# Optimization experiments

Measured on AMD Instinct MI355X. Metric: run time of the kernel, lower is better.

Reference implementation:

```python
import jax, jax.numpy as jnp
import numpy as np

OBS = 256      # observation_space_size == state_vector_len
SV = 2047      # STATE_VECTORS = WMG_MAX_OBS
D = 256        # tfm_vec_size = 8 heads * 32 head_size
H = 8
HD = 32
L = 2          # TFM_NUM_LAYERS
FF = 1024      # TFM_HIDDEN_SIZE
ACH = 512      # AC_HIDDEN_LAYER_SIZE
A = 16         # action_space_size


def setup_inputs() -> dict:
    key = jax.random.key(0)
    ks = jax.random.split(key, 24)
    r = lambda k, s: (jax.random.normal(k, s, jnp.float32) * 0.02)
    inp = {
        "observation": jax.random.normal(ks[0], (OBS,), jnp.float32),
        "old_vectors": jax.random.normal(ks[1], (SV, OBS), jnp.float32),
        "W_core": r(ks[2], (OBS, D)), "b_core": jnp.zeros((D,), jnp.float32),
        # memo embedding takes cat(state_vec, age_onehot) of size OBS+SV
        "W_memo": r(ks[3], (OBS + SV, D)), "b_memo": jnp.zeros((D,), jnp.float32),
        "Wq": r(ks[4], (L, D, D)), "bq": jnp.zeros((L, D), jnp.float32),
        "Wk": r(ks[5], (L, D, D)), "bk": jnp.zeros((L, D), jnp.float32),
        "Wv": r(ks[6], (L, D, D)), "bv": jnp.zeros((L, D), jnp.float32),
        "Wo": r(ks[7], (L, D, D)), "bo": jnp.zeros((L, D), jnp.float32),
        "ln1_g": jnp.ones((L, D), jnp.float32), "ln1_b": jnp.zeros((L, D), jnp.float32),
        "ln2_g": jnp.ones((L, D), jnp.float32), "ln2_b": jnp.zeros((L, D), jnp.float32),
        "W_ff1": r(ks[8], (L, D, FF)), "b_ff1": jnp.zeros((L, FF), jnp.float32),
        "W_ff2": r(ks[9], (L, FF, D)), "b_ff2": jnp.zeros((L, D), jnp.float32),
        "aW1": r(ks[10], (D, ACH)), "ab1": jnp.zeros((ACH,), jnp.float32),
        "aW2": r(ks[11], (ACH, ACH)), "ab2": jnp.zeros((ACH,), jnp.float32),
        "aWo": r(ks[12], (ACH, A)), "abo": jnp.zeros((A,), jnp.float32),
        "cW1": r(ks[13], (D, ACH)), "cb1": jnp.zeros((ACH,), jnp.float32),
        "cW2": r(ks[14], (ACH, ACH)), "cb2": jnp.zeros((ACH,), jnp.float32),
        "cWo": r(ks[15], (ACH, 1)), "cbo": jnp.zeros((1,), jnp.float32),
    }
    return inp


def _ln(x, g, b, eps=1e-5):
    m = jnp.mean(x, axis=-1, keepdims=True)
    v = jnp.mean(jnp.square(x - m), axis=-1, keepdims=True)
    return (x - m) * jax.lax.rsqrt(v + eps) * g + b


def reference(observation, old_vectors, W_core, b_core, W_memo, b_memo,
              Wq, bq, Wk, bk, Wv, bv, Wo, bo,
              ln1_g, ln1_b, ln2_g, ln2_b, W_ff1, b_ff1, W_ff2, b_ff2,
              aW1, ab1, aW2, ab2, aWo, abo, cW1, cb1, cW2, cb2, cWo, cbo):
    # core embedding [D]
    emb0 = observation @ W_core + b_core
    # fused memo + age-onehot embedding: cat(vec_i, e_i) @ W_memo == vec_i @ W_memo[:OBS] + W_memo[OBS+i]
    memo_emb = old_vectors @ W_memo[:OBS] + W_memo[OBS:] + b_memo  # [SV, D]
    x = jnp.concatenate([emb0[None, :], memo_emb], axis=0)[None]   # [1, 1+SV, D]
    S = 1 + SV
    scale = 1.0 / np.sqrt(HD).astype(np.float32)
    for l in range(L):
        q = (x @ Wq[l] + bq[l]).reshape(1, S, H, HD)
        k = (x @ Wk[l] + bk[l]).reshape(1, S, H, HD)
        v = (x @ Wv[l] + bv[l]).reshape(1, S, H, HD)
        scores = jnp.einsum('bqhd,bkhd->bhqk', q, k) * scale       # [1,H,S,S]
        probs = jax.nn.softmax(scores, axis=-1)
        ctx = jnp.einsum('bhqk,bkhd->bqhd', probs, v).reshape(1, S, D)
        x = _ln(x + ctx @ Wo[l] + bo[l], ln1_g[l], ln1_b[l])
        h = jax.nn.gelu(x @ W_ff1[l] + b_ff1[l])
        x = _ln(x + h @ W_ff2[l] + b_ff2[l], ln2_g[l], ln2_b[l])
    t = x[:, 0, :]                                                 # [1, D]
    ha = jnp.tanh(jnp.tanh(t @ aW1 + ab1) @ aW2 + ab2)
    policy = ha @ aWo + abo                                        # [1, A] logits
    hc = jnp.tanh(jnp.tanh(t @ cW1 + cb1) @ cW2 + cb2)
    value_est = hc @ cWo + cbo                                     # [1, 1]
    # WMG_MAX_MEMOS == 0 path: new state vector is tanh(observation)
    new_vector = jnp.tanh(observation)                             # [OBS]
    return value_est, policy, new_vector
```

## Files before the change

kernel.cpp:

```cpp
#include <hip/hip_runtime.h>
#include <stdint.h>

typedef __attribute__((ext_vector_type(8))) short bf16x8;
typedef __attribute__((ext_vector_type(4))) float f32x4;

constexpr int kSEQ = 2048;
constexpr int kD   = 256;
constexpr int kHD  = 32;
constexpr int kFF  = 1024;
constexpr int kA   = 16;

__device__ __forceinline__ unsigned short f2b(float f) {
  union { float f; unsigned int u; } v; v.f = f;
  unsigned int r = v.u + 0x7FFFu + ((v.u >> 16) & 1u);
  return (unsigned short)(r >> 16);
}

struct ConvTable {
  const float* src[13];
  int K[13];
  int N[13];
  int dst[13];
  int tstart[14];
};

union SharedU {
  struct { unsigned short lt[64][72]; } cv;
  struct { unsigned short Al[64][40]; unsigned short Bl[32][40]; } g64;
  struct { unsigned short Kl[64][40]; unsigned short Vt[32][72];
           unsigned short Pl[4][16][72]; } at;
};

struct MegaParams {
  ConvTable tab;
  const float *obs, *oldv, *Wcore, *bcore, *Wmemo0, *bmemo, *Wmemo2;
  const float *bq, *bk, *bv, *bo, *ln1g, *ln1b, *ln2g, *ln2b, *bff1, *bff2;
  const float *aW1, *ab1, *aW2, *ab2, *aWo, *abo;
  const float *cW1, *cb1, *cW2, *cb2, *cWo, *cbo;
  float* xf; unsigned short* xb;
  unsigned short *qb, *kb, *vb, *wT;
  float *pacc, *pml, *h1, *h2, *out;
  int oQKV[2], oWoT[2], oFF1[2], oFF2[2];
  int convJobs, nsplit, tpb;
};

__device__ void conv_job(const MegaParams& p, SharedU& sh, int job) {
  const int tid = threadIdx.x;
  if (job == p.convJobs) {
    float a = p.bcore[tid];
    #pragma unroll 8
    for (int k = 0; k < 256; k++) a += p.obs[k] * p.Wcore[k * kD + tid];
    p.xf[tid] = a;
    p.xb[tid] = f2b(a);
    return;
  }
  int m = 0;
  while (job >= p.tab.tstart[m + 1]) m++;
  const int tloc = job - p.tab.tstart[m];
  const int N = p.tab.N[m], K = p.tab.K[m];
  const int ntile = N >> 6;
  const int k0 = (tloc / ntile) * 64, n0 = (tloc % ntile) * 64;
  const float* src = p.tab.src[m];
  {
    const int r = tid >> 2, c16 = (tid & 3) * 16;
    const float* sp = src + (size_t)(k0 + r) * N + n0 + c16;
    #pragma unroll
    for (int j = 0; j < 16; j++) sh.cv.lt[r][c16 + j] = f2b(sp[j]);
  }
  __syncthreads();
  {
    const int n = tid >> 2, kc = (tid & 3) * 16;
    unsigned short* dp = p.wT + p.tab.dst[m] + (size_t)(n0 + n) * K + k0 + kc;
    unsigned short g[16];
    #pragma unroll
    for (int j = 0; j < 16; j++) g[j] = sh.cv.lt[kc + j][n];
    *(bf16x8*)dp = *(bf16x8*)&g[0];
    *(bf16x8*)(dp + 8) = *(bf16x8*)&g[8];
  }
}

__device__ void memo_job(const MegaParams& p, SharedU& sh, int job) {
  const int tid = threadIdx.x;
  const int w = tid >> 6, l = tid & 63, lg = l >> 4, lr = l & 15;
  const int sr = tid >> 2, sk = (tid & 3) * 8;
  const int kr = tid >> 3, nc = (tid & 7) * 4;
  const int m0 = (job & 31) * 64, n0 = (job >> 5) * 32;
  f32x4 acc[2];
  #pragma unroll
  for (int c = 0; c < 2; c++)
    #pragma unroll
    for (int i = 0; i < 4; i++) acc[c][i] = 0.f;

  auto loadA = [&](int k0) -> bf16x8 {
    bf16x8 av;
    if (m0 + sr < 2047) {
      const float* ap = p.oldv + (size_t)(m0 + sr) * 256 + k0 + sk;
      #pragma unroll
      for (int j = 0; j < 8; j++) av[j] = (short)f2b(ap[j]);
    } else {
      #pragma unroll
      for (int j = 0; j < 8; j++) av[j] = 0;
    }
    return av;
  };
  auto loadB = [&](int k0, float* b4) {
    const float* bp = p.Wmemo0 + (size_t)(k0 + kr) * kD + n0 + nc;
    #pragma unroll
    for (int j = 0; j < 4; j++) b4[j] = bp[j];
  };

  bf16x8 av = loadA(0);
  float b4[4];
  loadB(0, b4);

  for (int k0 = 0; k0 < 256; k0 += 32) {
    __syncthreads();
    *(bf16x8*)&sh.g64.Al[sr][sk] = av;
    #pragma unroll
    for (int j = 0; j < 4; j++) sh.g64.Bl[nc + j][kr] = f2b(b4[j]);
    __syncthreads();
    if (k0 + 32 < 256) {
      av = loadA(k0 + 32);
      loadB(k0 + 32, b4);
    }
    bf16x8 af = *(bf16x8*)&sh.g64.Al[w * 16 + lr][8 * lg];
    #pragma unroll
    for (int c = 0; c < 2; c++) {
      bf16x8 bf = *(bf16x8*)&sh.g64.Bl[c * 16 + lr][8 * lg];
      acc[c] = __builtin_amdgcn_mfma_f32_16x16x32_bf16(af, bf, acc[c], 0, 0, 0);
    }
  }

  #pragma unroll
  for (int c = 0; c < 2; c++)
    #pragma unroll
    for (int i = 0; i < 4; i++) {
      const int gr = m0 + w * 16 + 4 * lg + i;
      const int gc = n0 + c * 16 + lr;
      if (gr >= 2047) continue;
      const float v = acc[c][i] + p.bmemo[gc] + p.Wmemo2[(size_t)gr * kD + gc];
      p.xf[(size_t)(gr + 1) * kD + gc] = v;
      p.xb[(size_t)(gr + 1) * kD + gc] = f2b(v);
    }
}

__global__ __launch_bounds__(256) void k_cvm(MegaParams p) {
  __shared__ SharedU sh;
  if (blockIdx.x < 256) memo_job(p, sh, blockIdx.x);
  else conv_job(p, sh, blockIdx.x - 256);
}

__global__ __launch_bounds__(256) void k_qkv(MegaParams p, int lyr) {
  __shared__ SharedU sh;
  const int tid = threadIdx.x;
  const int w = tid >> 6, l = tid & 63, lg = l >> 4, lr = l & 15;
  const int sr = tid >> 2, sk = (tid & 3) * 8;
  const int job = blockIdx.x;
  const int m0 = (job & 31) * 64, n0 = (job >> 5) * 32;
  const unsigned short* BT = p.wT + p.oQKV[lyr];
  f32x4 acc[2];
  #pragma unroll
  for (int c = 0; c < 2; c++)
    #pragma unroll
    for (int i = 0; i < 4; i++) acc[c][i] = 0.f;

  bf16x8 av = *(const bf16x8*)(p.xb + (size_t)(m0 + sr) * 256 + sk);
  bf16x8 bv;
  if (tid < 128) bv = *(const bf16x8*)(BT + (size_t)(n0 + sr) * 256 + sk);

  for (int k0 = 0; k0 < 256; k0 += 32) {
    __syncthreads();
    *(bf16x8*)&sh.g64.Al[sr][sk] = av;
    if (tid < 128) *(bf16x8*)&sh.g64.Bl[sr][sk] = bv;
    __syncthreads();
    if (k0 + 32 < 256) {
      av = *(const bf16x8*)(p.xb + (size_t)(m0 + sr) * 256 + k0 + 32 + sk);
      if (tid < 128)
        bv = *(const bf16x8*)(BT + (size_t)(n0 + sr) * 256 + k0 + 32 + sk);
    }
    bf16x8 af = *(bf16x8*)&sh.g64.Al[w * 16 + lr][8 * lg];
    #pragma unroll
    for (int c = 0; c < 2; c++) {
      bf16x8 bf = *(bf16x8*)&sh.g64.Bl[c * 16 + lr][8 * lg];
      acc[c] = __builtin_amdgcn_mfma_f32_16x16x32_bf16(af, bf, acc[c], 0, 0, 0);
    }
  }

  #pragma unroll
  for (int c = 0; c < 2; c++)
    #pragma unroll
    for (int i = 0; i < 4; i++) {
      const int gr = m0 + w * 16 + 4 * lg + i;
      const int gc = n0 + c * 16 + lr;
      const int t = gc >> 8, cc = gc & 255;
      const float* bp = (t == 0) ? (p.bq + lyr * 256)
                        : (t == 1 ? (p.bk + lyr * 256) : (p.bv + lyr * 256));
      unsigned short* op = (t == 0) ? p.qb : (t == 1 ? p.kb : p.vb);
      float v = acc[c][i] + bp[cc];
      if (t == 0) v *= 0.17677669529663687f;
      op[(size_t)gr * kD + cc] = f2b(v);
    }
}

__device__ void attn_job(SharedU& sh, int qb_, int h, int s, int tpb,
                         const unsigned short* q, const unsigned short* k,
                         const unsigned short* v, float* pacc, float* pml) {
  const int tid = threadIdx.x;
  const int w = tid >> 6, l = tid & 63, lg = l >> 4, lr = l & 15;
  const int q0 = qb_ * 64;
  const int hoff = h * kHD;
  const int sr = tid >> 2, sk = (tid & 3) * 8;
  const int t0 = s * tpb;

  const bf16x8 qf =
      *(const bf16x8*)(q + (size_t)(q0 + w * 16 + lr) * kD + hoff + 8 * lg);

  float m_[4], l_[4];
  f32x4 acc[2];
  #pragma unroll
  for (int i = 0; i < 4; i++) { m_[i] = -1e30f; l_[i] = 0.f; }
  #pragma unroll
  for (int dt = 0; dt < 2; dt++)
    #pragma unroll
    for (int i = 0; i < 4; i++) acc[dt][i] = 0.f;

  bf16x8 kreg = *(const bf16x8*)(k + (size_t)(t0 * 64 + sr) * kD + hoff + sk);
  bf16x8 vreg = *(const bf16x8*)(v + (size_t)(t0 * 64 + sr) * kD + hoff + sk);

  for (int t = 0; t < tpb; t++) {
    __syncthreads();
    *(bf16x8*)&sh.at.Kl[sr][sk] = kreg;
    #pragma unroll
    for (int j = 0; j < 8; j++) sh.at.Vt[sk + j][sr] = (unsigned short)vreg[j];
    __syncthreads();
    if (t + 1 < tpb) {
      const size_t nx = (size_t)((t0 + t + 1) * 64 + sr) * kD + hoff + sk;
      kreg = *(const bf16x8*)(k + nx);
      vreg = *(const bf16x8*)(v + nx);
    }
    f32x4 sc[4];
    #pragma unroll
    for (int c = 0; c < 4; c++) {
      f32x4 z;
      #pragma unroll
      for (int i = 0; i < 4; i++) z[i] = 0.f;
      bf16x8 kf = *(bf16x8*)&sh.at.Kl[c * 16 + lr][8 * lg];
      sc[c] = __builtin_amdgcn_mfma_f32_16x16x32_bf16(qf, kf, z, 0, 0, 0);
    }
    float tm[4];
    #pragma unroll
    for (int i = 0; i < 4; i++)
      tm[i] = fmaxf(fmaxf(sc[0][i], sc[1][i]), fmaxf(sc[2][i], sc[3][i]));
    #pragma unroll
    for (int mm = 1; mm <= 8; mm <<= 1)
      #pragma unroll
      for (int i = 0; i < 4; i++) tm[i] = fmaxf(tm[i], __shfl_xor(tm[i], mm));
    float pv[4][4], rs[4], corr[4];
    #pragma unroll
    for (int i = 0; i < 4; i++) {
      const float nm = fmaxf(m_[i], tm[i]);
      corr[i] = __expf(m_[i] - nm);
      m_[i] = nm;
      rs[i] = 0.f;
    }
    #pragma unroll
    for (int c = 0; c < 4; c++)
      #pragma unroll
      for (int i = 0; i < 4; i++) {
        pv[c][i] = __expf(sc[c][i] - m_[i]);
        rs[i] += pv[c][i];
      }
    #pragma unroll
    for (int mm = 1; mm <= 8; mm <<= 1)
      #pragma unroll
      for (int i = 0; i < 4; i++) rs[i] += __shfl_xor(rs[i], mm);
    #pragma unroll
    for (int i = 0; i < 4; i++) {
      l_[i] = l_[i] * corr[i] + rs[i];
      acc[0][i] *= corr[i];
      acc[1][i] *= corr[i];
    }
    #pragma unroll
    for (int c = 0; c < 4; c++)
      #pragma unroll
      for (int i = 0; i < 4; i++)
        sh.at.Pl[w][4 * lg + i][c * 16 + lr] = f2b(pv[c][i]);
    __syncthreads();
    #pragma unroll
    for (int k2 = 0; k2 < 2; k2++) {
      bf16x8 pf_ = *(bf16x8*)&sh.at.Pl[w][lr][k2 * 32 + 8 * lg];
      #pragma unroll
      for (int dt = 0; dt < 2; dt++) {
        bf16x8 vf = *(bf16x8*)&sh.at.Vt[dt * 16 + lr][k2 * 32 + 8 * lg];
        acc[dt] = __builtin_amdgcn_mfma_f32_16x16x32_bf16(pf_, vf, acc[dt], 0, 0, 0);
      }
    }
  }

  const int pb = s * 8 + h;
  float* pa = pacc + (size_t)pb * kSEQ * kHD;
  float* pm = pml + (size_t)pb * kSEQ * 2;
  #pragma unroll
  for (int dt = 0; dt < 2; dt++)
    #pragma unroll
    for (int i = 0; i < 4; i++) {
      const int gr = q0 + w * 16 + 4 * lg + i;
      pa[(size_t)gr * kHD + dt * 16 + lr] = acc[dt][i];
    }
  if (lr == 0) {
    #pragma unroll
    for (int i = 0; i < 4; i++) {
      const int gr = q0 + w * 16 + 4 * lg + i;
      float2 ml; ml.x = m_[i]; ml.y = l_[i];
      *(float2*)&pm[(size_t)gr * 2] = ml;
    }
  }
}

__global__ __launch_bounds__(256) void k_attn(MegaParams p) {
  __shared__ SharedU sh;
  const int job = blockIdx.x;
  const int qb_ = job & 31, h = (job >> 5) & 7, s = job >> 8;
  attn_job(sh, qb_, h, s, p.tpb, p.qb, p.kb, p.vb, p.pacc, p.pml);
}

__device__ __forceinline__ void ln16w(float v[4], float2 (*red)[16],
                                      const float* gam, const float* bet,
                                      int ww, int lg, int lr) {
  float ps[4], ps2[4];
  #pragma unroll
  for (int i = 0; i < 4; i++) { ps[i] = v[i]; ps2[i] = v[i] * v[i]; }
  #pragma unroll
  for (int mm = 1; mm <= 8; mm <<= 1)
    #pragma unroll
    for (int i = 0; i < 4; i++) {
      ps[i] += __shfl_xor(ps[i], mm);
      ps2[i] += __shfl_xor(ps2[i], mm);
    }
  if (lr == 0) {
    #pragma unroll
    for (int i = 0; i < 4; i++) {
      float2 t; t.x = ps[i]; t.y = ps2[i];
      red[ww][4 * lg + i] = t;
    }
  }
  __syncthreads();
  #pragma unroll
  for (int i = 0; i < 4; i++) {
    const int ri = 4 * lg + i;
    float sx = 0.f, sx2 = 0.f;
    #pragma unroll
    for (int w2 = 0; w2 < 16; w2++) {
      float2 t = red[w2][ri];
      sx += t.x; sx2 += t.y;
    }
    const float mean = sx * (1.0f / 256.0f);
    const float var = sx2 * (1.0f / 256.0f) - mean * mean;
    const float rstd = rsqrtf(var + 1e-5f);
    const int col = ww * 16 + lr;
    v[i] = (v[i] - mean) * rstd * gam[col] + bet[col];
  }
}

__device__ __forceinline__ f32x4 gemm16(const bf16x8 a_[8],
                                        const unsigned short* Brow, int ldb,
                                        f32x4 acc, int lg) {
  bf16x8 b_[8];
  #pragma unroll
  for (int k8 = 0; k8 < 8; k8++)
    b_[k8] = *(const bf16x8*)(Brow + k8 * 32 + 8 * lg);
  #pragma unroll
  for (int k8 = 0; k8 < 8; k8++)
    acc = __builtin_amdgcn_mfma_f32_16x16x32_bf16(a_[k8], b_[k8], acc, 0, 0, 0);
  return acc;
}

template <bool QKV, int NSPLIT>
__global__ __launch_bounds__(1024) void k_block(MegaParams p, int lyr) {
  __shared__ unsigned short As[16][264];
  __shared__ unsigned short Hs[16][1032];
  __shared__ float2 red[16][16];
  const int tid = threadIdx.x;
  const int ww = tid >> 6, l = tid & 63, lg = l >> 4, lr = l & 15;
  const int r0 = blockIdx.x * 16;

  {
    const int row = r0 + (tid >> 6);
    const int kc = (tid & 63) * 4;
    const int h_ = kc >> 5;
    const int d0 = kc & 31;
    float pmx[NSPLIT], pll[NSPLIT];
    #pragma unroll
    for (int s2 = 0; s2 < NSPLIT; s2++) {
      const float2 t =
          *(const float2*)&p.pml[((size_t)(s2 * 8 + h_) * kSEQ + row) * 2];
      pmx[s2] = t.x; pll[s2] = t.y;
    }
    f32x4 pa_[NSPLIT];
    #pragma unroll
    for (int s2 = 0; s2 < NSPLIT; s2++)
      pa_[s2] = *(const f32x4*)(p.pacc +
                                ((size_t)(s2 * 8 + h_) * kSEQ + row) * kHD + d0);
    float mx = -1e30f;
    #pragma unroll
    for (int s2 = 0; s2 < NSPLIT; s2++) mx = fmaxf(mx, pmx[s2]);
    float L = 0.f;
    float o[4] = {0.f, 0.f, 0.f, 0.f};
    #pragma unroll
    for (int s2 = 0; s2 < NSPLIT; s2++) {
      const float es = __expf(pmx[s2] - mx);
      L += pll[s2] * es;
      #pragma unroll
      for (int j = 0; j < 4; j++) o[j] += pa_[s2][j] * es;
    }
    const float inv = 1.0f / L;
    unsigned short* dst = &As[tid >> 6][kc];
    #pragma unroll
    for (int j = 0; j < 4; j++) dst[j] = f2b(o[j] * inv);
  }
  __syncthreads();

  float yv[4];
  {
    bf16x8 a_[8];
    #pragma unroll
    for (int k8 = 0; k8 < 8; k8++)
      a_[k8] = *(bf16x8*)&As[lr][k8 * 32 + 8 * lg];
    f32x4 acc = {0.f, 0.f, 0.f, 0.f};
    acc = gemm16(a_, p.wT + p.oWoT[lyr] + (size_t)(ww * 16 + lr) * 256, 256,
                 acc, lg);
    const float* bias = p.bo + lyr * kD;
    const int col = ww * 16 + lr;
    #pragma unroll
    for (int i = 0; i < 4; i++) {
      const int gr = r0 + 4 * lg + i;
      yv[i] = acc[i] + bias[col] + p.xf[(size_t)gr * kD + col];
    }
    ln16w(yv, red, p.ln1g + lyr * kD, p.ln1b + lyr * kD, ww, lg, lr);
    __syncthreads();
    #pragma unroll
    for (int i = 0; i < 4; i++)
      As[4 * lg + i][col] = f2b(yv[i]);
  }
  __syncthreads();

  {
    bf16x8 a_[8];
    #pragma unroll
    for (int k8 = 0; k8 < 8; k8++)
      a_[k8] = *(bf16x8*)&As[lr][k8 * 32 + 8 * lg];
    const unsigned short* BT = p.wT + p.oFF1[lyr];
    const float* bias = p.bff1 + lyr * kFF;
    #pragma unroll
    for (int ct = 0; ct < 4; ct++) {
      f32x4 acc = {0.f, 0.f, 0.f, 0.f};
      acc = gemm16(a_, BT + (size_t)(ww * 64 + ct * 16 + lr) * 256, 256, acc, lg);
      const int col = ww * 64 + ct * 16 + lr;
      #pragma unroll
      for (int i = 0; i < 4; i++) {
        const float v = acc[i] + bias[col];
        const float u = 0.7978845608028654f * (v + 0.044715f * v * v * v);
        const float g = v / (1.0f + __expf(-2.0f * u));
        Hs[4 * lg + i][col] = f2b(g);
      }
    }
  }
  __syncthreads();

  float zv[4];
  {
    const unsigned short* Brow = p.wT + p.oFF2[lyr] + (size_t)(ww * 16 + lr) * 1024;
    f32x4 acc = {0.f, 0.f, 0.f, 0.f};
    #pragma unroll
    for (int kc = 0; kc < 4; kc++) {
      bf16x8 a_[8];
      #pragma unroll
      for (int k8 = 0; k8 < 8; k8++)
        a_[k8] = *(bf16x8*)&Hs[lr][kc * 256 + k8 * 32 + 8 * lg];
      acc = gemm16(a_, Brow + kc * 256, 1024, acc, lg);
    }
    const float* bias = p.bff2 + lyr * kD;
    const int col = ww * 16 + lr;
    #pragma unroll
    for (int i = 0; i < 4; i++) zv[i] = acc[i] + bias[col] + yv[i];
    ln16w(zv, red, p.ln2g + lyr * kD, p.ln2b + lyr * kD, ww, lg, lr);
    #pragma unroll
    for (int i = 0; i < 4; i++) {
      const int gr = r0 + 4 * lg + i;
      p.xf[(size_t)gr * kD + col] = zv[i];
      p.xb[(size_t)gr * kD + col] = f2b(zv[i]);
      if constexpr (QKV) As[4 * lg + i][col] = f2b(zv[i]);
    }
  }

  if constexpr (QKV) {
    __syncthreads();
    bf16x8 a_[8];
    #pragma unroll
    for (int k8 = 0; k8 < 8; k8++)
      a_[k8] = *(bf16x8*)&As[lr][k8 * 32 + 8 * lg];
    const unsigned short* BT = p.wT + p.oQKV[lyr + 1];
    const float* bq_ = p.bq + (lyr + 1) * 256;
    const float* bk_ = p.bk + (lyr + 1) * 256;
    const float* bv_ = p.bv + (lyr + 1) * 256;
    #pragma unroll
    for (int t = 0; t < 3; t++) {
      f32x4 acc = {0.f, 0.f, 0.f, 0.f};
      acc = gemm16(a_, BT + (size_t)(ww * 48 + t * 16 + lr) * 256, 256, acc, lg);
      const int gc = ww * 48 + t * 16 + lr;
      const int tb = gc >> 8, cc = gc & 255;
      const float* bp = (tb == 0) ? bq_ : (tb == 1 ? bk_ : bv_);
      unsigned short* op = (tb == 0) ? p.qb : (tb == 1 ? p.kb : p.vb);
      #pragma unroll
      for (int i = 0; i < 4; i++) {
        const int gr = r0 + 4 * lg + i;
        float v = acc[i] + bp[cc];
        if (tb == 0) v *= 0.17677669529663687f;
        op[(size_t)gr * kD + cc] = f2b(v);
      }
    }
  }
}

__global__ __launch_bounds__(256) void k_h1(MegaParams p) {
  __shared__ float tl[256];
  __shared__ float red[4][64];
  const int tid = threadIdx.x;
  tl[tid] = p.xf[tid];
  __syncthreads();
  const int jj = blockIdx.x * 64;
  const bool actor = jj < 512;
  const float* W = actor ? p.aW1 : p.cW1;
  const float* b = actor ? p.ab1 : p.cb1;
  const int j0 = actor ? jj : jj - 512;
  const int ks = tid >> 6, j = tid & 63;
  float s = 0.f;
  #pragma unroll 4
  for (int k2 = ks * 64; k2 < ks * 64 + 64; k2++)
    s += tl[k2] * W[(size_t)k2 * 512 + j0 + j];
  red[ks][j] = s;
  __syncthreads();
  if (tid < 64) {
    float t = red[0][tid] + red[1][tid] + red[2][tid] + red[3][tid] + b[j0 + tid];
    p.h1[jj + tid] = tanhf(t);
  }
}

__global__ __launch_bounds__(256) void k_h2(MegaParams p) {
  __shared__ float tl[512];
  __shared__ float red[4][64];
  const int tid = threadIdx.x;
  const int jj = blockIdx.x * 64;
  const bool actor = jj < 512;
  const float* hin = actor ? p.h1 : p.h1 + 512;
  tl[tid] = hin[tid];
  tl[tid + 256] = hin[tid + 256];
  __syncthreads();
  const float* W = actor ? p.aW2 : p.cW2;
  const float* b = actor ? p.ab2 : p.cb2;
  const int j0 = actor ? jj : jj - 512;
  const int ks = tid >> 6, j = tid & 63;
  float s = 0.f;
  #pragma unroll 4
  for (int k2 = ks * 128; k2 < ks * 128 + 128; k2++)
    s += tl[k2] * W[(size_t)k2 * 512 + j0 + j];
  red[ks][j] = s;
  __syncthreads();
  if (tid < 64) {
    float t = red[0][tid] + red[1][tid] + red[2][tid] + red[3][tid] + b[j0 + tid];
    p.h2[jj + tid] = tanhf(t);
  }
}

__global__ __launch_bounds__(256) void k_h3(MegaParams p) {
  __shared__ float ha[512], hc[512], vred[4];
  const int tid = threadIdx.x;
  ha[tid] = p.h2[tid];
  ha[tid + 256] = p.h2[tid + 256];
  hc[tid] = p.h2[512 + tid];
  hc[tid + 256] = p.h2[768 + tid];
  __syncthreads();
  const int g = tid >> 4, l16 = tid & 15;
  float s = 0.f;
  for (int k2 = l16 * 32; k2 < l16 * 32 + 32; k2++)
    s += ha[k2] * p.aWo[(size_t)k2 * kA + g];
  #pragma unroll
  for (int mm = 1; mm <= 8; mm <<= 1) s += __shfl_xor(s, mm);
  if (l16 == 0) p.out[1 + g] = s + p.abo[g];
  float vv = hc[tid] * p.cWo[tid] + hc[tid + 256] * p.cWo[tid + 256];
  #pragma unroll
  for (int mm = 1; mm <= 32; mm <<= 1) vv += __shfl_xor(vv, mm);
  if ((tid & 63) == 0) vred[tid >> 6] = vv;
  __syncthreads();
  if (tid == 0)
    p.out[0] = vred[0] + vred[1] + vred[2] + vred[3] + p.cbo[0];
  p.out[17 + tid] = tanhf(p.obs[tid]);
}

extern "C" void kernel_launch(void* const* d_in, const int* in_sizes, int n_in,
                              void* d_out, int out_size, void* d_ws, size_t ws_size,
                              hipStream_t stream) {
  const float* obs   = (const float*)d_in[0];
  const float* oldv  = (const float*)d_in[1];
  const float* Wcore = (const float*)d_in[2];
  const float* bcore = (const float*)d_in[3];
  const float* Wmemo = (const float*)d_in[4];
  const float* bmemo = (const float*)d_in[5];
  const float* Wq    = (const float*)d_in[6];
  const float* bq    = (const float*)d_in[7];
  const float* Wk    = (const float*)d_in[8];
  const float* bk    = (const float*)d_in[9];
  const float* Wv    = (const float*)d_in[10];
  const float* bv    = (const float*)d_in[11];
  const float* Wo    = (const float*)d_in[12];
  const float* bo    = (const float*)d_in[13];
  const float* ln1g  = (const float*)d_in[14];
  const float* ln1b  = (const float*)d_in[15];
  const float* ln2g  = (const float*)d_in[16];
  const float* ln2b  = (const float*)d_in[17];
  const float* Wff1  = (const float*)d_in[18];
  const float* bff1  = (const float*)d_in[19];
  const float* Wff2  = (const float*)d_in[20];
  const float* bff2  = (const float*)d_in[21];

  MegaParams P;
  P.obs = obs; P.oldv = oldv; P.Wcore = Wcore; P.bcore = bcore;
  P.Wmemo0 = Wmemo; P.bmemo = bmemo; P.Wmemo2 = Wmemo + 256 * 256;
  P.bq = bq; P.bk = bk; P.bv = bv; P.bo = bo;
  P.ln1g = ln1g; P.ln1b = ln1b; P.ln2g = ln2g; P.ln2b = ln2b;
  P.bff1 = bff1; P.bff2 = bff2;
  P.aW1 = (const float*)d_in[22]; P.ab1 = (const float*)d_in[23];
  P.aW2 = (const float*)d_in[24]; P.ab2 = (const float*)d_in[25];
  P.aWo = (const float*)d_in[26]; P.abo = (const float*)d_in[27];
  P.cW1 = (const float*)d_in[28]; P.cb1 = (const float*)d_in[29];
  P.cW2 = (const float*)d_in[30]; P.cb2 = (const float*)d_in[31];
  P.cWo = (const float*)d_in[32]; P.cbo = (const float*)d_in[33];

  char* ws = (char*)d_ws;
  P.xf = (float*)(ws + 0);
  P.xb = (unsigned short*)(ws + (2u << 20));
  P.qb = (unsigned short*)(ws + (3u << 20));
  P.kb = (unsigned short*)(ws + (4u << 20));
  P.vb = (unsigned short*)(ws + (5u << 20));
  P.wT = (unsigned short*)(ws + (6u << 20));
  P.h1 = (float*)(ws + (10u << 20));
  P.h2 = (float*)(ws + (10u << 20) + 8192);
  P.out = (float*)d_out;

  int nsplit = 8;
  const size_t paccOff = (size_t)14u << 20;
  const size_t pmlOff  = (size_t)31u << 20;
  while (nsplit > 1 &&
         (paccOff + (size_t)nsplit * 8 * kSEQ * kHD * 4 > pmlOff ||
          pmlOff + (size_t)nsplit * 8 * kSEQ * 2 * 4 > ws_size))
    nsplit >>= 1;
  P.pacc = (float*)(ws + paccOff);
  P.pml  = (float*)(ws + pmlOff);
  P.nsplit = nsplit;
  P.tpb = 32 / nsplit;

  int cur = 0;
  for (int l2 = 0; l2 < 2; l2++) {
    P.oQKV[l2] = cur; cur += 196608;
    P.oWoT[l2] = cur; cur += 65536;
    P.oFF1[l2] = cur; cur += 262144;
    P.oFF2[l2] = cur; cur += 262144;
  }

  int idx = 0, ts = 0;
  auto add = [&](const float* s, int K, int N, int dst) {
    P.tab.src[idx] = s; P.tab.K[idx] = K; P.tab.N[idx] = N;
    P.tab.dst[idx] = dst; P.tab.tstart[idx] = ts;
    ts += (K >> 6) * (N >> 6); idx++;
  };
  for (int l2 = 0; l2 < 2; l2++) {
    add(Wq + l2 * 65536, 256, 256, P.oQKV[l2]);
    add(Wk + l2 * 65536, 256, 256, P.oQKV[l2] + 65536);
    add(Wv + l2 * 65536, 256, 256, P.oQKV[l2] + 131072);
    add(Wo + l2 * 65536, 256, 256, P.oWoT[l2]);
    add(Wff1 + l2 * 262144, 256, 1024, P.oFF1[l2]);
    add(Wff2 + l2 * 262144, 1024, 256, P.oFF2[l2]);
  }
  P.tab.tstart[idx] = ts;
  P.convJobs = ts;

  auto launch_block = [&](bool qkv, int lyr) {
    if (qkv) {
      switch (nsplit) {
        case 8: k_block<true, 8><<<128, 1024, 0, stream>>>(P, lyr); break;
        case 4: k_block<true, 4><<<128, 1024, 0, stream>>>(P, lyr); break;
        case 2: k_block<true, 2><<<128, 1024, 0, stream>>>(P, lyr); break;
        default: k_block<true, 1><<<128, 1024, 0, stream>>>(P, lyr); break;
      }
    } else {
      switch (nsplit) {
        case 8: k_block<false, 8><<<128, 1024, 0, stream>>>(P, lyr); break;
        case 4: k_block<false, 4><<<128, 1024, 0, stream>>>(P, lyr); break;
        case 2: k_block<false, 2><<<128, 1024, 0, stream>>>(P, lyr); break;
        default: k_block<false, 1><<<128, 1024, 0, stream>>>(P, lyr); break;
      }
    }
  };

  k_cvm<<<256 + ts + 1, 256, 0, stream>>>(P);
  k_qkv<<<768, 256, 0, stream>>>(P, 0);
  k_attn<<<256 * nsplit, 256, 0, stream>>>(P);
  launch_block(true, 0);
  k_attn<<<256 * nsplit, 256, 0, stream>>>(P);
  launch_block(false, 1);
  k_h1<<<16, 256, 0, stream>>>(P);
  k_h2<<<16, 256, 0, stream>>>(P);
  k_h3<<<1, 256, 0, stream>>>(P);
}
```

Baseline: 200.5 us.

## Stage weight tiles through double-buffered LDS in block GEMMs

Adds a shared gemm_stage helper that has all 1024 threads cooperatively load 256x32 bf16 weight chunks into a double-buffered LDS tile, prefetching the next chunk while computing the current one. Every GEMM in the block kernel (Wo, FF1, FF2, QKV) now reads weight fragments from LDS instead of each wave loading its own strided rows from global memory. The aim is coalesced weight traffic. The cost is a block-wide barrier per 32-wide k chunk, only one chunk in flight at a time, and about 36KB of extra LDS, which could expose more global-load latency than the old batch of eight independent loads per wave.

```diff
diff --git a/kernel.cpp b/kernel.cpp
--- a/kernel.cpp
+++ b/kernel.cpp
@@ -362,16 +362,26 @@
   }
 }
 
-__device__ __forceinline__ f32x4 gemm16(const bf16x8 a_[8],
-                                        const unsigned short* Brow, int ldb,
-                                        f32x4 acc, int lg) {
-  bf16x8 b_[8];
-  #pragma unroll
-  for (int k8 = 0; k8 < 8; k8++)
-    b_[k8] = *(const bf16x8*)(Brow + k8 * 32 + 8 * lg);
-  #pragma unroll
-  for (int k8 = 0; k8 < 8; k8++)
-    acc = __builtin_amdgcn_mfma_f32_16x16x32_bf16(a_[k8], b_[k8], acc, 0, 0, 0);
+__device__ __forceinline__ f32x4 gemm_stage(
+    int nchunks, const unsigned short* __restrict__ BT, int ldb, int nbase,
+    const unsigned short* __restrict__ Abase, int astr,
+    unsigned short (*Bst)[36], int tid, int ww, int lg, int lr) {
+  const int sn = tid >> 2, sk = (tid & 3) * 8;
+  const unsigned short* Bsrc = BT + (size_t)(nbase + sn) * ldb + sk;
+  f32x4 acc = {0.f, 0.f, 0.f, 0.f};
+  bf16x8 bv = *(const bf16x8*)Bsrc;
+  *(bf16x8*)&Bst[sn][sk] = bv;
+  __syncthreads();
+  for (int kk = 0; kk < nchunks; kk++) {
+    if (kk + 1 < nchunks)
+      bv = *(const bf16x8*)(Bsrc + (kk + 1) * 32);
+    bf16x8 af = *(const bf16x8*)(Abase + (size_t)lr * astr + kk * 32 + 8 * lg);
+    bf16x8 bf = *(const bf16x8*)&Bst[(kk & 1) * 256 + ww * 16 + lr][8 * lg];
+    acc = __builtin_amdgcn_mfma_f32_16x16x32_bf16(af, bf, acc, 0, 0, 0);
+    if (kk + 1 < nchunks)
+      *(bf16x8*)&Bst[((kk + 1) & 1) * 256 + sn][sk] = bv;
+    __syncthreads();
+  }
   return acc;
 }
 
@@ -379,6 +389,7 @@
 __global__ __launch_bounds__(1024) void k_block(MegaParams p, int lyr) {
   __shared__ unsigned short As[16][264];
   __shared__ unsigned short Hs[16][1032];
+  __shared__ unsigned short Bst[512][36];
   __shared__ float2 red[16][16];
   const int tid = threadIdx.x;
   const int ww = tid >> 6, l = tid & 63, lg = l >> 4, lr = l & 15;
@@ -422,13 +433,8 @@
 
   float yv[4];
   {
-    bf16x8 a_[8];
-    #pragma unroll
-    for (int k8 = 0; k8 < 8; k8++)
-      a_[k8] = *(bf16x8*)&As[lr][k8 * 32 + 8 * lg];
-    f32x4 acc = {0.f, 0.f, 0.f, 0.f};
-    acc = gemm16(a_, p.wT + p.oWoT[lyr] + (size_t)(ww * 16 + lr) * 256, 256,
-                 acc, lg);
+    f32x4 acc = gemm_stage(8, p.wT + p.oWoT[lyr], 256, 0, &As[0][0], 264,
+                           Bst, tid, ww, lg, lr);
     const float* bias = p.bo + lyr * kD;
     const int col = ww * 16 + lr;
     #pragma unroll
@@ -445,17 +451,12 @@
   __syncthreads();
 
   {
-    bf16x8 a_[8];
-    #pragma unroll
-    for (int k8 = 0; k8 < 8; k8++)
-      a_[k8] = *(bf16x8*)&As[lr][k8 * 32 + 8 * lg];
     const unsigned short* BT = p.wT + p.oFF1[lyr];
     const float* bias = p.bff1 + lyr * kFF;
-    #pragma unroll
-    for (int ct = 0; ct < 4; ct++) {
-      f32x4 acc = {0.f, 0.f, 0.f, 0.f};
-      acc = gemm16(a_, BT + (size_t)(ww * 64 + ct * 16 + lr) * 256, 256, acc, lg);
-      const int col = ww * 64 + ct * 16 + lr;
+    for (int ng = 0; ng < 4; ng++) {
+      f32x4 acc = gemm_stage(8, BT, 256, ng * 256, &As[0][0], 264,
+                             Bst, tid, ww, lg, lr);
+      const int col = ng * 256 + ww * 16 + lr;
       #pragma unroll
       for (int i = 0; i < 4; i++) {
         const float v = acc[i] + bias[col];
@@ -469,16 +470,8 @@
 
   float zv[4];
   {
-    const unsigned short* Brow = p.wT + p.oFF2[lyr] + (size_t)(ww * 16 + lr) * 1024;
-    f32x4 acc = {0.f, 0.f, 0.f, 0.f};
-    #pragma unroll
-    for (int kc = 0; kc < 4; kc++) {
-      bf16x8 a_[8];
-      #pragma unroll
-      for (int k8 = 0; k8 < 8; k8++)
-        a_[k8] = *(bf16x8*)&Hs[lr][kc * 256 + k8 * 32 + 8 * lg];
-      acc = gemm16(a_, Brow + kc * 256, 1024, acc, lg);
-    }
+    f32x4 acc = gemm_stage(32, p.wT + p.oFF2[lyr], 1024, 0, &Hs[0][0], 1032,
+                           Bst, tid, ww, lg, lr);
     const float* bias = p.bff2 + lyr * kD;
     const int col = ww * 16 + lr;
     #pragma unroll
@@ -495,27 +488,20 @@
 
   if constexpr (QKV) {
     __syncthreads();
-    bf16x8 a_[8];
-    #pragma unroll
-    for (int k8 = 0; k8 < 8; k8++)
-      a_[k8] = *(bf16x8*)&As[lr][k8 * 32 + 8 * lg];
     const unsigned short* BT = p.wT + p.oQKV[lyr + 1];
-    const float* bq_ = p.bq + (lyr + 1) * 256;
-    const float* bk_ = p.bk + (lyr + 1) * 256;
-    const float* bv_ = p.bv + (lyr + 1) * 256;
-    #pragma unroll
-    for (int t = 0; t < 3; t++) {
-      f32x4 acc = {0.f, 0.f, 0.f, 0.f};
-      acc = gemm16(a_, BT + (size_t)(ww * 48 + t * 16 + lr) * 256, 256, acc, lg);
-      const int gc = ww * 48 + t * 16 + lr;
-      const int tb = gc >> 8, cc = gc & 255;
-      const float* bp = (tb == 0) ? bq_ : (tb == 1 ? bk_ : bv_);
-      unsigned short* op = (tb == 0) ? p.qb : (tb == 1 ? p.kb : p.vb);
+    for (int ng = 0; ng < 3; ng++) {
+      f32x4 acc = gemm_stage(8, BT, 256, ng * 256, &As[0][0], 264,
+                             Bst, tid, ww, lg, lr);
+      const int cc = ww * 16 + lr;
+      const float* bp = (ng == 0) ? (p.bq + (lyr + 1) * 256)
+                        : (ng == 1 ? (p.bk + (lyr + 1) * 256)
+                                   : (p.bv + (lyr + 1) * 256));
+      unsigned short* op = (ng == 0) ? p.qb : (ng == 1 ? p.kb : p.vb);
       #pragma unroll
       for (int i = 0; i < 4; i++) {
         const int gr = r0 + 4 * lg + i;
         float v = acc[i] + bp[cc];
-        if (tb == 0) v *= 0.17677669529663687f;
+        if (ng == 0) v *= 0.17677669529663687f;
         op[(size_t)gr * kD + cc] = f2b(v);
       }
     }
```

After: 296.0 us. 47.7% more time.
